# Performance work log

Measured on AMD Instinct MI355X. Metric: run time of the kernel, lower is better.

## Reference

```python
import jax, jax.numpy as jnp
import numpy as np

S, C1, C2, N = 4096, 2048, 2048, 1024


def setup_inputs() -> dict:
    key = jax.random.key(0)
    k1, k2, k3, k4 = jax.random.split(key, 4)
    # child log-likelihoods (samples, child_nodes); modest scale so exp() stays finite,
    # matching the (numerically naive) torch forward which exps without max-subtraction.
    ll1 = jax.random.normal(k1, (S, C1), dtype=jnp.float32)
    ll2 = jax.random.normal(k2, (S, C2), dtype=jnp.float32)
    # log edge weights, one tensor per child layer: (nodes, child_nodes)
    w1 = jax.random.normal(k3, (N, C1), dtype=jnp.float32)
    w2 = jax.random.normal(k4, (N, C2), dtype=jnp.float32)
    return {"ll1": ll1, "ll2": ll2, "w1": w1, "w2": w2}


def reference(ll1, ll2, w1, w2):
    # Per child layer: sum_c exp(ll[s,c] + w[n,c]) == exp(ll) @ exp(w).T  -> (S, N)
    # (same math as unsqueeze/repeat/exp/sum in the torch code, without the (S,C,N) blowup)
    result = jnp.exp(ll1) @ jnp.exp(w1).T + jnp.exp(ll2) @ jnp.exp(w2).T  # (S, N)
    # per-node log normalization constant over concatenated weights
    log_z = jax.nn.logsumexp(jnp.concatenate([w1, w2], axis=1), axis=1)  # (N,)
    return jnp.log(result) - log_z[None, :]
```

## Files before the change

### kernel.cpp

```cpp
#include <hip/hip_runtime.h>

#define S_DIM 4096
#define C_DIM 2048
#define N_DIM 1024
#define K_DIM 4096

#define BM2 256
#define BN2 256
#define KS 4
#define KSL (K_DIM / KS)
#define BK 32
#define NT2 (KSL / BK)
#define TILE2 32768
#define NBUF2 4

#define BM1 128
#define BN1 128
#define NT1 (K_DIM / BK)
#define TILE1 16384
#define NBUF1 8

typedef __attribute__((ext_vector_type(8))) short bf16x8;
typedef __attribute__((ext_vector_type(8))) unsigned short u16x8;
typedef __attribute__((ext_vector_type(4))) float f32x4;

__device__ static inline unsigned short f2bf(float f) {
    unsigned int u = __float_as_uint(f);
    u += 0x7FFFu + ((u >> 16) & 1u);
    return (unsigned short)(u >> 16);
}
__device__ static inline float bf2f(unsigned short h) {
    return __uint_as_float((unsigned int)h << 16);
}

__global__ void exp_ll_kernel(const float* __restrict__ ll1,
                              const float* __restrict__ ll2,
                              unsigned short* __restrict__ A) {
    const int total4 = S_DIM * C_DIM / 4;
    int stride = gridDim.x * blockDim.x;
    for (int i = blockIdx.x * blockDim.x + threadIdx.x; i < total4; i += stride) {
        int e = i << 2;
        int r = e >> 11;
        int c = e & 2047;
        size_t dst = ((size_t)r << 12) + c;
        float4 v = *reinterpret_cast<const float4*>(ll1 + e);
        ushort4 o;
        o.x = f2bf(__expf(v.x)); o.y = f2bf(__expf(v.y));
        o.z = f2bf(__expf(v.z)); o.w = f2bf(__expf(v.w));
        *reinterpret_cast<ushort4*>(A + dst) = o;
        float4 u = *reinterpret_cast<const float4*>(ll2 + e);
        ushort4 p;
        p.x = f2bf(__expf(u.x)); p.y = f2bf(__expf(u.y));
        p.z = f2bf(__expf(u.z)); p.w = f2bf(__expf(u.w));
        *reinterpret_cast<ushort4*>(A + dst + C_DIM) = p;
    }
}

__global__ void w_kernel(const float* __restrict__ w1,
                         const float* __restrict__ w2,
                         unsigned short* __restrict__ B,
                         float* __restrict__ lz) {
    const int n = blockIdx.x;
    const int tid = threadIdx.x;
    const int lane = tid & 63, wv = tid >> 6;
    const float* r1 = w1 + ((size_t)n << 11);
    const float* r2 = w2 + ((size_t)n << 11);
    float4 v0 = *reinterpret_cast<const float4*>(r1 + tid * 8);
    float4 v1 = *reinterpret_cast<const float4*>(r1 + tid * 8 + 4);
    float4 u0 = *reinterpret_cast<const float4*>(r2 + tid * 8);
    float4 u1 = *reinterpret_cast<const float4*>(r2 + tid * 8 + 4);

    float mx = fmaxf(fmaxf(fmaxf(v0.x, v0.y), fmaxf(v0.z, v0.w)),
                     fmaxf(fmaxf(v1.x, v1.y), fmaxf(v1.z, v1.w)));
    mx = fmaxf(mx, fmaxf(fmaxf(fmaxf(u0.x, u0.y), fmaxf(u0.z, u0.w)),
                          fmaxf(fmaxf(u1.x, u1.y), fmaxf(u1.z, u1.w))));
    #pragma unroll
    for (int off = 32; off > 0; off >>= 1) mx = fmaxf(mx, __shfl_xor(mx, off));
    __shared__ float red[4];
    if (lane == 0) red[wv] = mx;
    __syncthreads();
    mx = fmaxf(fmaxf(red[0], red[1]), fmaxf(red[2], red[3]));

    float s = __expf(v0.x - mx) + __expf(v0.y - mx) + __expf(v0.z - mx) + __expf(v0.w - mx)
            + __expf(v1.x - mx) + __expf(v1.y - mx) + __expf(v1.z - mx) + __expf(v1.w - mx)
            + __expf(u0.x - mx) + __expf(u0.y - mx) + __expf(u0.z - mx) + __expf(u0.w - mx)
            + __expf(u1.x - mx) + __expf(u1.y - mx) + __expf(u1.z - mx) + __expf(u1.w - mx);
    #pragma unroll
    for (int off = 32; off > 0; off >>= 1) s += __shfl_xor(s, off);
    __shared__ float red2[4];
    if (lane == 0) red2[wv] = s;
    __syncthreads();
    if (tid == 0)
        lz[n] = mx + __logf(red2[0] + red2[1] + red2[2] + red2[3]);

    unsigned short* brow = B + ((size_t)n << 12);
    ushort4 o;
    o.x = f2bf(__expf(v0.x)); o.y = f2bf(__expf(v0.y));
    o.z = f2bf(__expf(v0.z)); o.w = f2bf(__expf(v0.w));
    *reinterpret_cast<ushort4*>(brow + tid * 8) = o;
    o.x = f2bf(__expf(v1.x)); o.y = f2bf(__expf(v1.y));
    o.z = f2bf(__expf(v1.z)); o.w = f2bf(__expf(v1.w));
    *reinterpret_cast<ushort4*>(brow + tid * 8 + 4) = o;
    o.x = f2bf(__expf(u0.x)); o.y = f2bf(__expf(u0.y));
    o.z = f2bf(__expf(u0.z)); o.w = f2bf(__expf(u0.w));
    *reinterpret_cast<ushort4*>(brow + C_DIM + tid * 8) = o;
    o.x = f2bf(__expf(u1.x)); o.y = f2bf(__expf(u1.y));
    o.z = f2bf(__expf(u1.z)); o.w = f2bf(__expf(u1.w));
    *reinterpret_cast<ushort4*>(brow + C_DIM + tid * 8 + 4) = o;
}

typedef const unsigned int __attribute__((address_space(1)))* gas_ptr;
typedef unsigned int __attribute__((address_space(3)))* las_ptr;

__global__ __launch_bounds__(512, 1) void gemm_split_kernel(
        const unsigned short* __restrict__ A,
        const unsigned short* __restrict__ B,
        unsigned short* __restrict__ P) {
    __shared__ __align__(16) char lds[NBUF2 * TILE2];
    const int tid  = threadIdx.x;
    const int l    = tid & 63;
    const int w    = tid >> 6;
    const int wg   = blockIdx.x;
    const int x7   = wg & 7;
    const int bm   = (wg >> 3) & 15;
    const int c    = x7 + ((wg >> 7) << 3);
    const int ks   = c >> 2;
    const int bn   = c & 3;
    const int wr = w >> 1, wc = w & 1;
    const int lcol = l & 15, lk = l >> 4;

    const int kg = (l & 3) ^ ((l >> 3) & 3);
    const unsigned short* src[4];
    int dst[4];
    #pragma unroll
    for (int i = 0; i < 4; ++i) {
        const int ri  = w + i * 8;
        const int row = ri * 16 + (l >> 2);
        src[i] = (i < 2)
            ? A + (size_t)(bm * BM2 + row) * K_DIM + ks * KSL + kg * 8
            : B + (size_t)(bn * BN2 + row - 256) * K_DIM + ks * KSL + kg * 8;
        dst[i] = row * 64 + (l & 3) * 16;
    }

    const int swz = (lk ^ ((lcol >> 1) & 3)) << 4;
    int aoff[4], boff[8];
    #pragma unroll
    for (int m = 0; m < 4; ++m) aoff[m] = (wr * 64 + m * 16 + lcol) * 64 + swz;
    #pragma unroll
    for (int n = 0; n < 8; ++n) boff[n] = 16384 + (wc * 128 + n * 16 + lcol) * 64 + swz;

    f32x4 acc[4][8] = {};
    bf16x8 a[4], b[8];

#define GLOAD(p_, o_) __builtin_amdgcn_global_load_lds((gas_ptr)(const void*)(p_), \
        (las_ptr)(void*)(lds + (o_)), 16, 0, 0)
#define STAGE2(T, BUFI) { const int _ko = (T) * BK; const int _bo = (BUFI) * TILE2; \
        GLOAD(src[0] + _ko, _bo + dst[0]); GLOAD(src[1] + _ko, _bo + dst[1]);       \
        GLOAD(src[2] + _ko, _bo + dst[2]); GLOAD(src[3] + _ko, _bo + dst[3]); }
#define READF2(RBUF) { const char* _rb = lds + (RBUF) * TILE2;                      \
        _Pragma("unroll") for (int m = 0; m < 4; ++m)                               \
            a[m] = *reinterpret_cast<const bf16x8*>(_rb + aoff[m]);                 \
        _Pragma("unroll") for (int n = 0; n < 8; ++n)                               \
            b[n] = *reinterpret_cast<const bf16x8*>(_rb + boff[n]); }
#define MFMAS2() {                                                                  \
        __builtin_amdgcn_s_setprio(1);                                              \
        _Pragma("unroll") for (int m = 0; m < 4; ++m)                               \
            _Pragma("unroll") for (int n = 0; n < 8; ++n)                           \
                acc[m][n] = __builtin_amdgcn_mfma_f32_16x16x32_bf16(a[m], b[n],     \
                                                                    acc[m][n], 0, 0, 0); \
        __builtin_amdgcn_s_setprio(0); }
#define BODY2(RBUF, TS, SBUF, WAITN, DOSTAGE) {                                     \
        asm volatile("s_waitcnt vmcnt(" #WAITN ")" ::: "memory");                   \
        __builtin_amdgcn_s_barrier();                                               \
        if (DOSTAGE) STAGE2(TS, SBUF);                                              \
        READF2(RBUF);                                                               \
        MFMAS2(); }

    STAGE2(0, 0); STAGE2(1, 1); STAGE2(2, 2);
    for (int t4 = 0; t4 < NT2 - 4; t4 += 4) {
        BODY2(0, t4 + 3, 3, 8, 1);
        BODY2(1, t4 + 4, 0, 8, 1);
        BODY2(2, t4 + 5, 1, 8, 1);
        BODY2(3, t4 + 6, 2, 8, 1);
    }
    BODY2(0, 31, 3, 8, 1);
    BODY2(1, 0, 0, 8, 0);
    BODY2(2, 0, 0, 4, 0);
    BODY2(3, 0, 0, 0, 0);
#undef BODY2
#undef MFMAS2
#undef READF2
#undef STAGE2

    unsigned short* Pk = P + (size_t)ks * ((size_t)S_DIM * N_DIM);
    const int col_base = bn * BN2 + wc * 128;
    #pragma unroll
    for (int m = 0; m < 4; ++m) {
        const int row0 = bm * BM2 + wr * 64 + m * 16 + lk * 4;
        #pragma unroll
        for (int n = 0; n < 8; ++n) {
            const int col = col_base + n * 16 + lcol;
            #pragma unroll
            for (int j = 0; j < 4; ++j)
                Pk[(size_t)(row0 + j) * N_DIM + col] = f2bf(acc[m][n][j]);
        }
    }
#undef GLOAD
}

__global__ void reduce_kernel(const unsigned short* __restrict__ P,
                              const float* __restrict__ lz,
                              float* __restrict__ out) {
    const size_t SN = (size_t)S_DIM * N_DIM;
    int i = blockIdx.x * blockDim.x + threadIdx.x;
    size_t e = (size_t)i * 8;
    int n = (int)(e & (N_DIM - 1));
    u16x8 p0 = *reinterpret_cast<const u16x8*>(P + e);
    u16x8 p1 = *reinterpret_cast<const u16x8*>(P + SN + e);
    u16x8 p2 = *reinterpret_cast<const u16x8*>(P + 2 * SN + e);
    u16x8 p3 = *reinterpret_cast<const u16x8*>(P + 3 * SN + e);
    float4 lz0 = *reinterpret_cast<const float4*>(lz + n);
    float4 lz1 = *reinterpret_cast<const float4*>(lz + n + 4);
    float lzv[8] = {lz0.x, lz0.y, lz0.z, lz0.w, lz1.x, lz1.y, lz1.z, lz1.w};
    float o[8];
    #pragma unroll
    for (int j = 0; j < 8; ++j) {
        float s = bf2f((unsigned short)p0[j]) + bf2f((unsigned short)p1[j])
                + bf2f((unsigned short)p2[j]) + bf2f((unsigned short)p3[j]);
        o[j] = __logf(s) - lzv[j];
    }
    *reinterpret_cast<float4*>(out + e)     = make_float4(o[0], o[1], o[2], o[3]);
    *reinterpret_cast<float4*>(out + e + 4) = make_float4(o[4], o[5], o[6], o[7]);
}

__global__ __launch_bounds__(256, 1) void gemm_log_kernel128(
        const unsigned short* __restrict__ A,
        const unsigned short* __restrict__ B,
        const float* __restrict__ lz,
        float* __restrict__ out) {
    __shared__ __align__(16) char lds[NBUF1 * TILE1];
    const int tid  = threadIdx.x;
    const int l    = tid & 63;
    const int w    = tid >> 6;
    const int bn = blockIdx.x & 7;
    const int bm = blockIdx.x >> 3;
    const int wr = w >> 1, wc = w & 1;
    const int lcol = l & 15, lk = l >> 4;

    const int kg = (l & 3) ^ ((l >> 3) & 3);
    const unsigned short* src[4];
    int dst[4];
    #pragma unroll
    for (int i = 0; i < 4; ++i) {
        const int ri  = w * 4 + i;
        const int row = ri * 16 + (l >> 2);
        src[i] = (ri < 8)
            ? A + (size_t)(bm * BM1 + row) * K_DIM + kg * 8
            : B + (size_t)(bn * BN1 + row - 128) * K_DIM + kg * 8;
        dst[i] = row * 64 + (l & 3) * 16;
    }
    const int swz = (lk ^ ((lcol >> 1) & 3)) << 4;
    int aoff[4], boff[4];
    #pragma unroll
    for (int m = 0; m < 4; ++m) aoff[m] = (wr * 64 + m * 16 + lcol) * 64 + swz;
    #pragma unroll
    for (int n = 0; n < 4; ++n) boff[n] = 8192 + (wc * 64 + n * 16 + lcol) * 64 + swz;

    f32x4 acc[4][4] = {};
    bf16x8 a0[4], b0[4], a1[4], b1[4];

#define GLOAD(p_, o_) __builtin_amdgcn_global_load_lds((gas_ptr)(const void*)(p_), \
        (las_ptr)(void*)(lds + (o_)), 16, 0, 0)
#define STAGE(T, BUFI) { const int _ko = (T) * BK; const int _bo = (BUFI) * TILE1; \
        GLOAD(src[0] + _ko, _bo + dst[0]); GLOAD(src[1] + _ko, _bo + dst[1]);      \
        GLOAD(src[2] + _ko, _bo + dst[2]); GLOAD(src[3] + _ko, _bo + dst[3]); }
#define READF(RBUF, AR, BR) { const char* _rb = lds + (RBUF) * TILE1;              \
        _Pragma("unroll") for (int m = 0; m < 4; ++m)                              \
            AR[m] = *reinterpret_cast<const bf16x8*>(_rb + aoff[m]);               \
        _Pragma("unroll") for (int n = 0; n < 4; ++n)                              \
            BR[n] = *reinterpret_cast<const bf16x8*>(_rb + boff[n]); }
#define MFMAS(AMM, BMM)                                                            \
        _Pragma("unroll") for (int m = 0; m < 4; ++m)                              \
            _Pragma("unroll") for (int n = 0; n < 4; ++n)                          \
                acc[m][n] = __builtin_amdgcn_mfma_f32_16x16x32_bf16(AMM[m], BMM[n],\
                                                                    acc[m][n], 0, 0, 0);
#define BODY(T, SB, RB, WAITN, DOSTAGE, AR, BR, AMM, BMM) {                        \
        asm volatile("s_waitcnt vmcnt(" #WAITN ")" ::: "memory");                  \
        __builtin_amdgcn_s_barrier();                                              \
        if (DOSTAGE) STAGE((T) + 8, SB);                                           \
        READF(RB, AR, BR);                                                         \
        MFMAS(AMM, BMM); }

    STAGE(0, 0); STAGE(1, 1); STAGE(2, 2); STAGE(3, 3);
    STAGE(4, 4); STAGE(5, 5); STAGE(6, 6); STAGE(7, 7);
    asm volatile("s_waitcnt vmcnt(28)" ::: "memory");
    __builtin_amdgcn_s_barrier();
    READF(0, a0, b0);
    for (int t8 = 0; t8 < NT1 - 8; t8 += 8) {
        BODY(t8 + 0, 0, 1, 24, 1, a1, b1, a0, b0);
        BODY(t8 + 1, 1, 2, 24, 1, a0, b0, a1, b1);
        BODY(t8 + 2, 2, 3, 24, 1, a1, b1, a0, b0);
        BODY(t8 + 3, 3, 4, 24, 1, a0, b0, a1, b1);
        BODY(t8 + 4, 4, 5, 24, 1, a1, b1, a0, b0);
        BODY(t8 + 5, 5, 6, 24, 1, a0, b0, a1, b1);
        BODY(t8 + 6, 6, 7, 24, 1, a1, b1, a0, b0);
        BODY(t8 + 7, 7, 0, 24, 1, a0, b0, a1, b1);
    }
    BODY(120, 0, 1, 24, 0, a1, b1, a0, b0);
    BODY(121, 1, 2, 20, 0, a0, b0, a1, b1);
    BODY(122, 2, 3, 16, 0, a1, b1, a0, b0);
    BODY(123, 3, 4, 12, 0, a0, b0, a1, b1);
    BODY(124, 4, 5,  8, 0, a1, b1, a0, b0);
    BODY(125, 5, 6,  4, 0, a0, b0, a1, b1);
    BODY(126, 6, 7,  0, 0, a1, b1, a0, b0);
    MFMAS(a1, b1);
#undef BODY
#undef MFMAS
#undef READF
#undef STAGE
#undef GLOAD

    const int col_base = bn * BN1 + wc * 64;
    float lzv[4];
    #pragma unroll
    for (int n = 0; n < 4; ++n) lzv[n] = lz[col_base + n * 16 + lcol];
    #pragma unroll
    for (int m = 0; m < 4; ++m) {
        const int row0 = bm * BM1 + wr * 64 + m * 16 + lk * 4;
        #pragma unroll
        for (int n = 0; n < 4; ++n) {
            const int col = col_base + n * 16 + lcol;
            #pragma unroll
            for (int j = 0; j < 4; ++j)
                out[(size_t)(row0 + j) * N_DIM + col] = __logf(acc[m][n][j]) - lzv[n];
        }
    }
}

__global__ void naive_kernel(const float* __restrict__ ll1, const float* __restrict__ ll2,
                             const float* __restrict__ w1, const float* __restrict__ w2,
                             float* __restrict__ out) {
    int idx = blockIdx.x * blockDim.x + threadIdx.x;
    if (idx >= S_DIM * N_DIM) return;
    int s = idx >> 10, n = idx & (N_DIM - 1);
    const float* a1 = ll1 + (size_t)s * C_DIM;
    const float* a2 = ll2 + (size_t)s * C_DIM;
    const float* b1 = w1 + (size_t)n * C_DIM;
    const float* b2 = w2 + (size_t)n * C_DIM;
    float mx = -3.0e38f;
    for (int c = 0; c < C_DIM; ++c) mx = fmaxf(mx, b1[c]);
    for (int c = 0; c < C_DIM; ++c) mx = fmaxf(mx, b2[c]);
    float zs = 0.f, acc = 0.f;
    for (int c = 0; c < C_DIM; ++c) { zs += __expf(b1[c] - mx); acc += __expf(a1[c] + b1[c]); }
    for (int c = 0; c < C_DIM; ++c) { zs += __expf(b2[c] - mx); acc += __expf(a2[c] + b2[c]); }
    out[idx] = __logf(acc) - (mx + __logf(zs));
}

extern "C" void kernel_launch(void* const* d_in, const int* in_sizes, int n_in,
                              void* d_out, int out_size, void* d_ws, size_t ws_size,
                              hipStream_t stream) {
    const float* ll1 = (const float*)d_in[0];
    const float* ll2 = (const float*)d_in[1];
    const float* w1  = (const float*)d_in[2];
    const float* w2  = (const float*)d_in[3];
    float* out = (float*)d_out;

    const size_t a_elems = (size_t)S_DIM * K_DIM;
    const size_t b_elems = (size_t)N_DIM * K_DIM;
    const size_t sn      = (size_t)S_DIM * N_DIM;
    const size_t need1 = (a_elems + b_elems) * sizeof(unsigned short) + N_DIM * sizeof(float);
    const size_t need2 = need1 + KS * sn * sizeof(unsigned short);
    if (ws_size < need1) {
        naive_kernel<<<(S_DIM * N_DIM + 255) / 256, 256, 0, stream>>>(ll1, ll2, w1, w2, out);
        return;
    }
    unsigned short* Aws = (unsigned short*)d_ws;
    unsigned short* Bws = Aws + a_elems;
    float* lzws = (float*)(Bws + b_elems);

    exp_ll_kernel<<<2048, 256, 0, stream>>>(ll1, ll2, Aws);
    w_kernel<<<N_DIM, 256, 0, stream>>>(w1, w2, Bws, lzws);

    if (ws_size >= need2) {
        unsigned short* Pws = (unsigned short*)(lzws + N_DIM);
        gemm_split_kernel<<<(S_DIM / BM2) * (N_DIM / BN2) * KS, 512, 0, stream>>>(Aws, Bws, Pws);
        reduce_kernel<<<(int)(sn / 8 / 256), 256, 0, stream>>>(Pws, lzws, out);
    } else {
        gemm_log_kernel128<<<(S_DIM / BM1) * (N_DIM / BN1), 256, 0, stream>>>(Aws, Bws, lzws, out);
    }
}
```

Baseline: 73.67 us.

## Double-buffer LDS fragment reads in registers and request two blocks per CU

Restructures the split-K GEMM main loop so the A/B fragments for the next k-step are read from LDS into a second register set while MFMAs run on the current set. This hides LDS read latency behind matrix math. Wait counts are tightened to match the earlier consumption. Launch bounds now request two 512-thread blocks per CU, which sharply lowers the register budget. Together with the doubled fragment registers and the 128 accumulator values per thread, this risks heavy spilling, and the 128 KB LDS footprint may prevent a second block from fitting anyway.

```diff
diff --git a/kernel.cpp b/kernel.cpp
--- a/kernel.cpp
+++ b/kernel.cpp
@@ -112,7 +112,7 @@
 typedef const unsigned int __attribute__((address_space(1)))* gas_ptr;
 typedef unsigned int __attribute__((address_space(3)))* las_ptr;
 
-__global__ __launch_bounds__(512, 1) void gemm_split_kernel(
+__global__ __launch_bounds__(512, 2) void gemm_split_kernel(
         const unsigned short* __restrict__ A,
         const unsigned short* __restrict__ B,
         unsigned short* __restrict__ P) {
@@ -130,63 +130,59 @@
     const int lcol = l & 15, lk = l >> 4;
 
     const int kg = (l & 3) ^ ((l >> 3) & 3);
-    const unsigned short* src[4];
-    int dst[4];
-    #pragma unroll
-    for (int i = 0; i < 4; ++i) {
-        const int ri  = w + i * 8;
-        const int row = ri * 16 + (l >> 2);
-        src[i] = (i < 2)
-            ? A + (size_t)(bm * BM2 + row) * K_DIM + ks * KSL + kg * 8
-            : B + (size_t)(bn * BN2 + row - 256) * K_DIM + ks * KSL + kg * 8;
-        dst[i] = row * 64 + (l & 3) * 16;
-    }
+    const unsigned short* srcA0 = A + (size_t)(bm * BM2 + w * 16 + (l >> 2)) * K_DIM
+                                    + ks * KSL + kg * 8;
+    const unsigned short* srcA1 = srcA0 + (size_t)128 * K_DIM;
+    const unsigned short* srcB0 = B + (size_t)(bn * BN2 + w * 16 + (l >> 2)) * K_DIM
+                                    + ks * KSL + kg * 8;
+    const unsigned short* srcB1 = srcB0 + (size_t)128 * K_DIM;
+    const int dst0 = (w * 16 + (l >> 2)) * 64 + (l & 3) * 16;
 
     const int swz = (lk ^ ((lcol >> 1) & 3)) << 4;
-    int aoff[4], boff[8];
-    #pragma unroll
-    for (int m = 0; m < 4; ++m) aoff[m] = (wr * 64 + m * 16 + lcol) * 64 + swz;
-    #pragma unroll
-    for (int n = 0; n < 8; ++n) boff[n] = 16384 + (wc * 128 + n * 16 + lcol) * 64 + swz;
+    const int abase = (wr * 64 + lcol) * 64 + swz;
+    const int bbase = 16384 + (wc * 128 + lcol) * 64 + swz;
 
     f32x4 acc[4][8] = {};
-    bf16x8 a[4], b[8];
+    bf16x8 a0[4], b0[8], a1[4], b1[8];
 
 #define GLOAD(p_, o_) __builtin_amdgcn_global_load_lds((gas_ptr)(const void*)(p_), \
         (las_ptr)(void*)(lds + (o_)), 16, 0, 0)
-#define STAGE2(T, BUFI) { const int _ko = (T) * BK; const int _bo = (BUFI) * TILE2; \
-        GLOAD(src[0] + _ko, _bo + dst[0]); GLOAD(src[1] + _ko, _bo + dst[1]);       \
-        GLOAD(src[2] + _ko, _bo + dst[2]); GLOAD(src[3] + _ko, _bo + dst[3]); }
-#define READF2(RBUF) { const char* _rb = lds + (RBUF) * TILE2;                      \
-        _Pragma("unroll") for (int m = 0; m < 4; ++m)                               \
-            a[m] = *reinterpret_cast<const bf16x8*>(_rb + aoff[m]);                 \
-        _Pragma("unroll") for (int n = 0; n < 8; ++n)                               \
-            b[n] = *reinterpret_cast<const bf16x8*>(_rb + boff[n]); }
-#define MFMAS2() {                                                                  \
-        __builtin_amdgcn_s_setprio(1);                                              \
-        _Pragma("unroll") for (int m = 0; m < 4; ++m)                               \
-            _Pragma("unroll") for (int n = 0; n < 8; ++n)                           \
-                acc[m][n] = __builtin_amdgcn_mfma_f32_16x16x32_bf16(a[m], b[n],     \
+#define STAGE2(T, BUFI) { const int _ko = (T) * BK; const int _bo = (BUFI) * TILE2;  \
+        GLOAD(srcA0 + _ko, _bo + dst0);         GLOAD(srcA1 + _ko, _bo + dst0 + 8192); \
+        GLOAD(srcB0 + _ko, _bo + dst0 + 16384); GLOAD(srcB1 + _ko, _bo + dst0 + 24576); }
+#define READF2(RBUF, AR, BR) { const char* _rb = lds + (RBUF) * TILE2;               \
+        _Pragma("unroll") for (int m = 0; m < 4; ++m)                                \
+            AR[m] = *reinterpret_cast<const bf16x8*>(_rb + abase + m * 1024);        \
+        _Pragma("unroll") for (int n = 0; n < 8; ++n)                                \
+            BR[n] = *reinterpret_cast<const bf16x8*>(_rb + bbase + n * 1024); }
+#define MFMAS2(AMM, BMM) {                                                           \
+        __builtin_amdgcn_s_setprio(1);                                               \
+        _Pragma("unroll") for (int m = 0; m < 4; ++m)                                \
+            _Pragma("unroll") for (int n = 0; n < 8; ++n)                            \
+                acc[m][n] = __builtin_amdgcn_mfma_f32_16x16x32_bf16(AMM[m], BMM[n],  \
                                                                     acc[m][n], 0, 0, 0); \
         __builtin_amdgcn_s_setprio(0); }
-#define BODY2(RBUF, TS, SBUF, WAITN, DOSTAGE) {                                     \
-        asm volatile("s_waitcnt vmcnt(" #WAITN ")" ::: "memory");                   \
-        __builtin_amdgcn_s_barrier();                                               \
-        if (DOSTAGE) STAGE2(TS, SBUF);                                              \
-        READF2(RBUF);                                                               \
-        MFMAS2(); }
+#define BODY2(RBUF, TS, SBUF, WAITN, DOSTAGE, AR, BR, AMM, BMM) {                    \
+        asm volatile("s_waitcnt vmcnt(" #WAITN ")" ::: "memory");                    \
+        __builtin_amdgcn_s_barrier();                                                \
+        if (DOSTAGE) STAGE2(TS, SBUF);                                               \
+        READF2(RBUF, AR, BR);                                                        \
+        MFMAS2(AMM, BMM); }
 
     STAGE2(0, 0); STAGE2(1, 1); STAGE2(2, 2);
+    asm volatile("s_waitcnt vmcnt(8)" ::: "memory");
+    __builtin_amdgcn_s_barrier();
+    READF2(0, a0, b0);
     for (int t4 = 0; t4 < NT2 - 4; t4 += 4) {
-        BODY2(0, t4 + 3, 3, 8, 1);
-        BODY2(1, t4 + 4, 0, 8, 1);
-        BODY2(2, t4 + 5, 1, 8, 1);
-        BODY2(3, t4 + 6, 2, 8, 1);
-    }
-    BODY2(0, 31, 3, 8, 1);
-    BODY2(1, 0, 0, 8, 0);
-    BODY2(2, 0, 0, 4, 0);
-    BODY2(3, 0, 0, 0, 0);
+        BODY2(1, t4 + 3, 3, 4, 1, a1, b1, a0, b0);
+        BODY2(2, t4 + 4, 0, 4, 1, a0, b0, a1, b1);
+        BODY2(3, t4 + 5, 1, 4, 1, a1, b1, a0, b0);
+        BODY2(0, t4 + 6, 2, 4, 1, a0, b0, a1, b1);
+    }
+    BODY2(1, 31, 3, 4, 1, a1, b1, a0, b0);
+    BODY2(2, 0, 0, 4, 0, a0, b0, a1, b1);
+    BODY2(3, 0, 0, 0, 0, a1, b1, a0, b0);
+    MFMAS2(a1, b1);
 #undef BODY2
 #undef MFMAS2
 #undef READF2
```

Result: slower. 78.68 us (+6.8%).
